# Performance work log

Measured on AMD Instinct MI355X. Metric: run time of the kernel, lower is better.

The kernel has to match this reference:

```python
import jax, jax.numpy as jnp
import numpy as np

N_NODES = 50000
N_EDGES = 600000
IN_F = 128
OUT_F = 128
SMALL = max(IN_F // 10, 1)  # floor(128/10) = 12
D_K = np.sqrt(SMALL).astype(np.float32)


def setup_inputs() -> dict:
    key = jax.random.key(0)
    ks = jax.random.split(key, 10)
    node_data = jax.random.normal(ks[0], (N_NODES, IN_F), dtype=jnp.float32)
    src = jax.random.randint(ks[1], (N_EDGES,), 0, N_NODES, dtype=jnp.int32)
    dst = jax.random.randint(ks[2], (N_EDGES,), 0, N_NODES, dtype=jnp.int32)
    s_q = 1.0 / np.sqrt(IN_F)
    Wq = jax.random.uniform(ks[3], (SMALL, IN_F), jnp.float32, -s_q, s_q)
    bq = jax.random.uniform(ks[4], (SMALL,), jnp.float32, -s_q, s_q)
    Wk = jax.random.uniform(ks[5], (SMALL, IN_F), jnp.float32, -s_q, s_q)
    bk = jax.random.uniform(ks[6], (SMALL,), jnp.float32, -s_q, s_q)
    W1 = jax.random.uniform(ks[7], (OUT_F, IN_F), jnp.float32, -s_q, s_q)
    W2 = jax.random.uniform(ks[8], (OUT_F, IN_F), jnp.float32, -s_q, s_q)
    b2 = jax.random.uniform(ks[9], (OUT_F,), jnp.float32, -s_q, s_q)
    return {"node_data": node_data, "src": src, "dst": dst,
            "Wq": Wq, "bq": bq, "Wk": Wk, "bk": bk,
            "W1": W1, "W2": W2, "b2": b2}


def reference(node_data, src, dst, Wq, bq, Wk, bk, W1, W2, b2):
    N = node_data.shape[0]
    # dgl.add_self_loop: append (i, i) for every node -> each dst has >= 1 edge
    loops = jnp.arange(N, dtype=src.dtype)
    s = jnp.concatenate([src, loops])
    d = jnp.concatenate([dst, loops])

    # query = Tanh(Linear), key = Linear  (shapes [N, SMALL])
    q = jnp.tanh(node_data @ Wq.T + bq)
    k = node_data @ Wk.T + bk

    # per-edge score: sum(query[src] * key[dst]) / sqrt(small)
    scores = jnp.sum(q[s] * k[d], axis=1) / D_K  # [E]

    # softmax over incoming edges of each dst node (segment softmax)
    seg_max = jax.ops.segment_max(scores, d, num_segments=N)
    w = jnp.exp(scores - seg_max[d])
    seg_sum = jax.ops.segment_sum(w, d, num_segments=N)
    w = w / seg_sum[d]  # [E]

    # weighted scatter-aggregate of src node inputs -> [N, IN_F]
    att = jax.ops.segment_sum(w[:, None] * node_data[s], d, num_segments=N)

    # DeepSetLayer: layer1(node_data) + layer2(node attention)
    x = node_data @ W1.T + (att @ W2.T + b2)
    # per-row L2 ('fro' over dim=1) normalization, then ReLU
    x = x / jnp.linalg.norm(x, axis=1, keepdims=True)
    return jax.nn.relu(x)
```

## Files before the change

### kernel.cpp

```cpp
#include <hip/hip_runtime.h>
#include <hip/hip_bf16.h>
#include <math.h>
#include <stdint.h>


#define IN_F 128
#define SMALL 12
#define QK_PAD 16
#define SCAN_ITEMS 8
#define SCAN_CHUNK 2048

typedef __attribute__((ext_vector_type(8))) _Float16 half8;
typedef __attribute__((ext_vector_type(4))) float f32x4;

__device__ __forceinline__ float dot12(const float* __restrict__ qrow,
                                       float4 c0, float4 c1, float4 c2) {
    float4 a = ((const float4*)qrow)[0];
    float4 b = ((const float4*)qrow)[1];
    float4 c = ((const float4*)qrow)[2];
    return a.x*c0.x + a.y*c0.y + a.z*c0.z + a.w*c0.w
         + b.x*c1.x + b.y*c1.y + b.z*c1.z + b.w*c1.w
         + c.x*c2.x + c.y*c2.y + c.z*c2.z + c.w*c2.w;
}

__device__ __forceinline__ half8 ld_h8(const float* p) {
    float4 x0 = *(const float4*)p;
    float4 x1 = *(const float4*)(p + 4);
    half8 a;
    a[0] = (_Float16)x0.x; a[1] = (_Float16)x0.y;
    a[2] = (_Float16)x0.z; a[3] = (_Float16)x0.w;
    a[4] = (_Float16)x1.x; a[5] = (_Float16)x1.y;
    a[6] = (_Float16)x1.z; a[7] = (_Float16)x1.w;
    return a;
}

__global__ __launch_bounds__(256) void prep_kernel(
    const float* __restrict__ nd,
    const float* __restrict__ Wq, const float* __restrict__ bq,
    const float* __restrict__ Wk, const float* __restrict__ bk,
    const int* __restrict__ dst,
    const float* __restrict__ W1, const float* __restrict__ W2,
    float* __restrict__ q, float* __restrict__ kf,
    unsigned short* __restrict__ ndb, int* __restrict__ cnt,
    unsigned short* __restrict__ rank, unsigned short* __restrict__ Wc,
    int N, int E, int NBQK, int NBCNT)
{
    int t = threadIdx.x;
    int b = blockIdx.x;

    if (b < NBQK) {
        int wv = t >> 6;
        int lane = t & 63;
        int col = lane & 15;
        int quad = lane >> 4;
        int tbase = b * 64 + wv * 16;

        int arow = tbase + col;
        int rowc = (arow < N) ? arow : (N - 1);
        const float* ap = nd + (size_t)rowc * IN_F + quad * 8;
        unsigned short* np = ndb + (size_t)arow * IN_F + quad * 8;

        const float* w0 = ((col < 12) ? (Wq + (size_t)col * IN_F)
                                      : (Wk + (size_t)(col - 12) * IN_F)) + quad * 8;
        const float* w1 = Wk + (size_t)((col < 8) ? (col + 4) : 4) * IN_F + quad * 8;
        bool hasw1 = (col < 8);

        half8 zero = {};
        f32x4 acc0 = (f32x4)0.f, acc1 = (f32x4)0.f;
#pragma unroll
        for (int ks = 0; ks < 4; ks++) {
            int k0 = ks * 32;
            half8 a = ld_h8(ap + k0);
            if (arow < N) *(half8*)(np + k0) = a;
            half8 bb0 = ld_h8(w0 + k0);
            half8 bb1 = hasw1 ? ld_h8(w1 + k0) : zero;
            acc0 = __builtin_amdgcn_mfma_f32_16x16x32_f16(a, bb0, acc0, 0, 0, 0);
            acc1 = __builtin_amdgcn_mfma_f32_16x16x32_f16(a, bb1, acc1, 0, 0, 0);
        }
        float bias0 = (col < 12) ? bq[col] : bk[col - 12];
        float bias1 = (col < 8) ? bk[col + 4] : 0.f;
#pragma unroll
        for (int r = 0; r < 4; r++) {
            int node = tbase + quad * 4 + r;
            if (node < N) {
                float v0 = acc0[r] + bias0;
                if (col < 12) q[(size_t)node * QK_PAD + col] = tanhf(v0);
                else          kf[(size_t)node * QK_PAD + (col - 12)] = v0;
                if (hasw1)    kf[(size_t)node * QK_PAD + col + 4] = acc1[r] + bias1;
            }
        }
    } else if (b < NBQK + NBCNT) {
        int ET = E + N;
        int stride = NBCNT * 256;
        for (int i = (b - NBQK) * 256 + t; i < ET; i += stride) {
            int d = (i < E) ? dst[i] : (i - E);
            rank[i] = (unsigned short)atomicAdd(&cnt[d], 1);
        }
    } else {
        int idx = (b - NBQK - NBCNT) * 256 + t;
        int f = idx >> 8, k = idx & 255;
        float v = (k < 128) ? W1[f * 128 + k] : W2[f * 128 + (k - 128)];
        ((_Float16*)Wc)[idx] = (_Float16)v;
    }
}

__global__ __launch_bounds__(256) void scan_local_kernel(
    int* __restrict__ off, int* __restrict__ bsum, int N)
{
    __shared__ int tsum[256];
    int t = threadIdx.x;
    int base = blockIdx.x * SCAN_CHUNK + t * SCAN_ITEMS;
    int v[SCAN_ITEMS];
    int s = 0;
#pragma unroll
    for (int i = 0; i < SCAN_ITEMS; i++) {
        int idx = base + i;
        v[i] = (idx < N) ? off[idx] : 0;
        s += v[i];
    }
    tsum[t] = s;
    __syncthreads();
    for (int d = 1; d < 256; d <<= 1) {
        int x = (t >= d) ? tsum[t - d] : 0;
        __syncthreads();
        tsum[t] += x;
        __syncthreads();
    }
    int excl = (t == 0) ? 0 : tsum[t - 1];
#pragma unroll
    for (int i = 0; i < SCAN_ITEMS; i++) {
        int idx = base + i;
        if (idx < N) off[idx] = excl;
        excl += v[i];
    }
    if (t == 255) bsum[blockIdx.x] = tsum[255];
}

__global__ __launch_bounds__(256) void scan_add_kernel(
    int* __restrict__ off, const int* __restrict__ bsum, int N, int NB)
{
    __shared__ int pre2[2];
    int t = threadIdx.x;
    if (t == 0) {
        int p = 0, tot = 0;
        for (int i = 0; i < NB; i++) {
            int v = bsum[i];
            if (i < (int)blockIdx.x) p += v;
            tot += v;
        }
        pre2[0] = p; pre2[1] = tot;
    }
    __syncthreads();
    int add = pre2[0];
    if (blockIdx.x == 0 && t == 0) off[N] = pre2[1];

    int base = blockIdx.x * SCAN_CHUNK + t * SCAN_ITEMS;
#pragma unroll
    for (int i = 0; i < SCAN_ITEMS; i++) {
        int j = base + i;
        if (j < N) off[j] += add;
    }
}

__global__ __launch_bounds__(256) void scatter_kernel(
    const int* __restrict__ src, const int* __restrict__ dst,
    const int* __restrict__ off, const unsigned short* __restrict__ rank,
    unsigned short* __restrict__ esrc, int E, int N)
{
    int i = blockIdx.x * 256 + threadIdx.x;
    if (i >= E + N) return;
    int d, s;
    if (i < E) { d = dst[i]; s = src[i]; }
    else       { d = i - E; s = d; }
    esrc[off[d] + (int)rank[i]] = (unsigned short)s;
}

__global__ __launch_bounds__(256) void attn_kernel(
    const unsigned short* __restrict__ ndb, const float* __restrict__ q,
    const float* __restrict__ kf, const int* __restrict__ off,
    const unsigned short* __restrict__ esrc, float* __restrict__ att, int N)
{
    const float INVDK = 0.28867513459481287f;
    int t = threadIdx.x;
    int lane = t & 63;
    int l16 = lane & 15;
    int gbase = lane & 48;
    int wid = blockIdx.x * 16 + (t >> 4);
    if (wid >= N) return;

    int start = off[wid];
    int deg = off[wid + 1] - start;

    const float4* kp = (const float4*)(kf + (size_t)wid * QK_PAD);
    float4 c0 = kp[0], c1 = kp[1], c2 = kp[2];

    float acc[8];
#pragma unroll
    for (int j = 0; j < 8; j++) acc[j] = 0.f;
    float inv;

    const unsigned short* nb = ndb + l16 * 8;

#define ACCUM(hv, ww) do {                                                    \
        acc[0] += (ww) * (float)(hv)[0]; acc[1] += (ww) * (float)(hv)[1];     \
        acc[2] += (ww) * (float)(hv)[2]; acc[3] += (ww) * (float)(hv)[3];     \
        acc[4] += (ww) * (float)(hv)[4]; acc[5] += (ww) * (float)(hv)[5];     \
        acc[6] += (ww) * (float)(hv)[6]; acc[7] += (ww) * (float)(hv)[7];     \
    } while (0)

    if (deg <= 16) {
        int si = 0;
        if (l16 < deg) si = (int)esrc[start + l16];

        int r0 = __shfl(si, gbase | 0);
        int r1 = __shfl(si, gbase | 1);
        int r2 = __shfl(si, gbase | 2);
        int r3 = __shfl(si, gbase | 3);
        half8 v0 = *(const half8*)(nb + (size_t)r0 * IN_F);
        half8 v1 = *(const half8*)(nb + (size_t)r1 * IN_F);
        half8 v2 = *(const half8*)(nb + (size_t)r2 * IN_F);
        half8 v3 = *(const half8*)(nb + (size_t)r3 * IN_F);

        float sc = -INFINITY;
        if (l16 < deg)
            sc = dot12(q + (size_t)si * QK_PAD, c0, c1, c2) * INVDK;
        float m = sc;
#pragma unroll
        for (int o = 8; o > 0; o >>= 1) m = fmaxf(m, __shfl_xor(m, o));
        float w = (l16 < deg) ? __expf(sc - m) : 0.f;
        float ls = w;
#pragma unroll
        for (int o = 8; o > 0; o >>= 1) ls += __shfl_xor(ls, o);
        inv = 1.f / ls;

        float w0 = __shfl(w, gbase | 0);
        float w1 = __shfl(w, gbase | 1);
        float w2 = __shfl(w, gbase | 2);
        float w3 = __shfl(w, gbase | 3);
        ACCUM(v0, w0); ACCUM(v1, w1); ACCUM(v2, w2); ACCUM(v3, w3);

        int i = 4;
        for (; i + 4 <= deg; i += 4) {
            float u0 = __shfl(w, gbase | i);       int s0 = __shfl(si, gbase | i);
            float u1 = __shfl(w, gbase | (i + 1)); int s1 = __shfl(si, gbase | (i + 1));
            float u2 = __shfl(w, gbase | (i + 2)); int s2 = __shfl(si, gbase | (i + 2));
            float u3 = __shfl(w, gbase | (i + 3)); int s3 = __shfl(si, gbase | (i + 3));
            half8 x0 = *(const half8*)(nb + (size_t)s0 * IN_F);
            half8 x1 = *(const half8*)(nb + (size_t)s1 * IN_F);
            half8 x2 = *(const half8*)(nb + (size_t)s2 * IN_F);
            half8 x3 = *(const half8*)(nb + (size_t)s3 * IN_F);
            ACCUM(x0, u0); ACCUM(x1, u1); ACCUM(x2, u2); ACCUM(x3, u3);
        }
        for (; i < deg; i++) {
            float wi = __shfl(w, gbase | i);
            int ri = __shfl(si, gbase | i);
            half8 x = *(const half8*)(nb + (size_t)ri * IN_F);
            ACCUM(x, wi);
        }
    } else {
        float m = -INFINITY;
        for (int i = l16; i < deg; i += 16) {
            int s2 = (int)esrc[start + i];
            m = fmaxf(m, dot12(q + (size_t)s2 * QK_PAD, c0, c1, c2) * INVDK);
        }
#pragma unroll
        for (int o = 8; o > 0; o >>= 1) m = fmaxf(m, __shfl_xor(m, o));
        float ls = 0.f;
        for (int i = l16; i < deg; i += 16) {
            int s2 = (int)esrc[start + i];
            ls += __expf(dot12(q + (size_t)s2 * QK_PAD, c0, c1, c2) * INVDK - m);
        }
#pragma unroll
        for (int o = 8; o > 0; o >>= 1) ls += __shfl_xor(ls, o);
        inv = 1.f / ls;

        for (int base2 = 0; base2 < deg; base2 += 16) {
            int cnt2 = deg - base2; if (cnt2 > 16) cnt2 = 16;
            float w = 0.f; int si = 0;
            if (l16 < cnt2) {
                si = (int)esrc[start + base2 + l16];
                w = __expf(dot12(q + (size_t)si * QK_PAD, c0, c1, c2) * INVDK - m);
            }
            int i = 0;
            for (; i + 4 <= cnt2; i += 4) {
                float u0 = __shfl(w, gbase | i);       int s0 = __shfl(si, gbase | i);
                float u1 = __shfl(w, gbase | (i + 1)); int s1 = __shfl(si, gbase | (i + 1));
                float u2 = __shfl(w, gbase | (i + 2)); int s2 = __shfl(si, gbase | (i + 2));
                float u3 = __shfl(w, gbase | (i + 3)); int s3 = __shfl(si, gbase | (i + 3));
                half8 x0 = *(const half8*)(nb + (size_t)s0 * IN_F);
                half8 x1 = *(const half8*)(nb + (size_t)s1 * IN_F);
                half8 x2 = *(const half8*)(nb + (size_t)s2 * IN_F);
                half8 x3 = *(const half8*)(nb + (size_t)s3 * IN_F);
                ACCUM(x0, u0); ACCUM(x1, u1); ACCUM(x2, u2); ACCUM(x3, u3);
            }
            for (; i < cnt2; i++) {
                float wi = __shfl(w, gbase | i);
                int ri = __shfl(si, gbase | i);
                half8 x = *(const half8*)(nb + (size_t)ri * IN_F);
                ACCUM(x, wi);
            }
        }
    }
#undef ACCUM

    float* op = att + (size_t)wid * IN_F + l16 * 8;
    float4 s0, s1;
    s0.x = acc[0] * inv; s0.y = acc[1] * inv; s0.z = acc[2] * inv; s0.w = acc[3] * inv;
    s1.x = acc[4] * inv; s1.y = acc[5] * inv; s1.z = acc[6] * inv; s1.w = acc[7] * inv;
    *(float4*)op = s0;
    *(float4*)(op + 4) = s1;
}

__global__ __launch_bounds__(256) void final_kernel(
    const unsigned short* __restrict__ ndb, const float* __restrict__ nd,
    const float* __restrict__ att,
    const unsigned short* __restrict__ Wc, const float* __restrict__ b2,
    float* __restrict__ out, int N)
{
    int wv = threadIdx.x >> 6;
    int lane = threadIdx.x & 63;
    int col = lane & 15;
    int quad = lane >> 4;

    int arow = blockIdx.x * 64 + wv * 16 + col;
    int rowc = (arow < N) ? arow : (N - 1);
    const unsigned short* a0p = ndb + (size_t)rowc * IN_F + quad * 8;
    const float* a1p = ((arow < N) ? att : nd) + (size_t)rowc * IN_F + quad * 8;

    f32x4 acc[8];
#pragma unroll
    for (int i = 0; i < 8; i++) acc[i] = (f32x4)0.f;

#pragma unroll
    for (int ks = 0; ks < 8; ks++) {
        int k0 = ks * 32;
        half8 a;
        if (ks < 4) a = *(const half8*)(a0p + k0);
        else        a = ld_h8(a1p + (k0 - 128));
#pragma unroll
        for (int ft = 0; ft < 8; ft++) {
            int n = ft * 16 + col;
            half8 bb = *(const half8*)(Wc + (size_t)n * 256 + k0 + quad * 8);
            acc[ft] = __builtin_amdgcn_mfma_f32_16x16x32_f16(a, bb, acc[ft], 0, 0, 0);
        }
    }

    float bias[8];
#pragma unroll
    for (int ft = 0; ft < 8; ft++) bias[ft] = b2[ft * 16 + col];

#pragma unroll
    for (int r = 0; r < 4; r++) {
        int node = blockIdx.x * 64 + wv * 16 + quad * 4 + r;
        float v[8];
        float ps = 0.f;
#pragma unroll
        for (int ft = 0; ft < 8; ft++) {
            v[ft] = acc[ft][r] + bias[ft];
            ps += v[ft] * v[ft];
        }
        ps += __shfl_xor(ps, 1);
        ps += __shfl_xor(ps, 2);
        ps += __shfl_xor(ps, 4);
        ps += __shfl_xor(ps, 8);
        float rn = rsqrtf(ps);
        if (node < N) {
            float* op = out + (size_t)node * 128 + col;
#pragma unroll
            for (int ft = 0; ft < 8; ft++)
                op[ft * 16] = fmaxf(v[ft] * rn, 0.f);
        }
    }
}

static inline char* align_up(char* p, size_t a) {
    return (char*)(((uintptr_t)p + (a - 1)) & ~(uintptr_t)(a - 1));
}

extern "C" void kernel_launch(void* const* d_in, const int* in_sizes, int n_in,
                              void* d_out, int out_size, void* d_ws, size_t ws_size,
                              hipStream_t stream) {
    const float* node_data = (const float*)d_in[0];
    const int*   src       = (const int*)d_in[1];
    const int*   dst       = (const int*)d_in[2];
    const float* Wq        = (const float*)d_in[3];
    const float* bq        = (const float*)d_in[4];
    const float* Wk        = (const float*)d_in[5];
    const float* bk        = (const float*)d_in[6];
    const float* W1        = (const float*)d_in[7];
    const float* W2        = (const float*)d_in[8];
    const float* b2        = (const float*)d_in[9];
    float* out = (float*)d_out;

    int N = in_sizes[0] / IN_F;
    int E = in_sizes[1];
    int ET = E + N;
    int NB = (N + SCAN_CHUNK - 1) / SCAN_CHUNK;
    int NBQK = (N + 63) / 64;
    int NBCNT = 512;
    int NBCVT = 128;

    char* w = (char*)d_ws;
    float* q  = (float*)w;  w += (size_t)N * QK_PAD * sizeof(float);
    float* kf = (float*)w;  w += (size_t)N * QK_PAD * sizeof(float);
    w = align_up(w, 256);
    unsigned short* ndb = (unsigned short*)w;  w += (size_t)N * IN_F * sizeof(unsigned short);
    w = align_up(w, 256);
    unsigned short* Wc = (unsigned short*)w;  w += 128 * 256 * sizeof(unsigned short);
    int* off  = (int*)w;  w += (size_t)(N + 1) * sizeof(int);
    int* bsum = (int*)w;  w += 256 * sizeof(int);
    unsigned short* rank = (unsigned short*)w;  w += (size_t)ET * sizeof(unsigned short);
    w = align_up(w, 256);
    unsigned short* esrc = (unsigned short*)w;  w += (size_t)ET * sizeof(unsigned short);
    float* att = out;

    hipMemsetAsync(off, 0, (size_t)(N + 1) * sizeof(int), stream);

    prep_kernel<<<NBQK + NBCNT + NBCVT, 256, 0, stream>>>(
        node_data, Wq, bq, Wk, bk, dst, W1, W2,
        q, kf, ndb, off, rank, Wc, N, E, NBQK, NBCNT);
    scan_local_kernel<<<NB, 256, 0, stream>>>(off, bsum, N);
    scan_add_kernel<<<NB, 256, 0, stream>>>(off, bsum, N, NB);
    scatter_kernel<<<(ET + 255) / 256, 256, 0, stream>>>(src, dst, off, rank, esrc, E, N);
    attn_kernel<<<(N + 15) / 16, 256, 0, stream>>>(ndb, q, kf, off, esrc, att, N);
    final_kernel<<<(N + 63) / 64, 256, 0, stream>>>(ndb, node_data, att, Wc, b2, out, N);
}
```

Measured before the change: 221.5 us.

## Pad CSR segments to 8, batch neighbor gathers, store attention in fp16

Keeps per-node counts in a separate array and pads each CSR segment to a multiple of 8. This allows source indices to be read as aligned 8-wide vectors and row gathers to be issued 8 or 16 at a time, for degree up to 32. It also writes the attention aggregate to an fp16 workspace buffer when the workspace is large enough, which halves that intermediate's traffic and removes the fp32-to-fp16 conversion in the final GEMM. The cost is a larger esrc buffer, extra register pressure from the wide batched loads, and some added precision loss in the attention aggregate.

```diff
diff --git a/kernel.cpp b/kernel.cpp
--- a/kernel.cpp
+++ b/kernel.cpp
@@ -11,6 +11,7 @@
 #define SCAN_CHUNK 2048
 
 typedef __attribute__((ext_vector_type(8))) _Float16 half8;
+typedef __attribute__((ext_vector_type(8))) unsigned short ushort8;
 typedef __attribute__((ext_vector_type(4))) float f32x4;
 
 __device__ __forceinline__ float dot12(const float* __restrict__ qrow,
@@ -105,7 +106,8 @@
 }
 
 __global__ __launch_bounds__(256) void scan_local_kernel(
-    int* __restrict__ off, int* __restrict__ bsum, int N)
+    const int* __restrict__ cnt, int* __restrict__ off,
+    int* __restrict__ bsum, int N)
 {
     __shared__ int tsum[256];
     int t = threadIdx.x;
@@ -115,7 +117,7 @@
 #pragma unroll
     for (int i = 0; i < SCAN_ITEMS; i++) {
         int idx = base + i;
-        v[i] = (idx < N) ? off[idx] : 0;
+        v[i] = (idx < N) ? ((cnt[idx] + 7) & ~7) : 0;
         s += v[i];
     }
     tsum[t] = s;
@@ -178,7 +180,8 @@
 __global__ __launch_bounds__(256) void attn_kernel(
     const unsigned short* __restrict__ ndb, const float* __restrict__ q,
     const float* __restrict__ kf, const int* __restrict__ off,
-    const unsigned short* __restrict__ esrc, float* __restrict__ att, int N)
+    const int* __restrict__ cnt, const unsigned short* __restrict__ esrc,
+    void* __restrict__ attv, int att16, int N)
 {
     const float INVDK = 0.28867513459481287f;
     int t = threadIdx.x;
@@ -189,7 +192,7 @@
     if (wid >= N) return;
 
     int start = off[wid];
-    int deg = off[wid + 1] - start;
+    int deg = cnt[wid];
 
     const float4* kp = (const float4*)(kf + (size_t)wid * QK_PAD);
     float4 c0 = kp[0], c1 = kp[1], c2 = kp[2];
@@ -208,54 +211,80 @@
         acc[6] += (ww) * (float)(hv)[6]; acc[7] += (ww) * (float)(hv)[7];     \
     } while (0)
 
-    if (deg <= 16) {
-        int si = 0;
-        if (l16 < deg) si = (int)esrc[start + l16];
-
-        int r0 = __shfl(si, gbase | 0);
-        int r1 = __shfl(si, gbase | 1);
-        int r2 = __shfl(si, gbase | 2);
-        int r3 = __shfl(si, gbase | 3);
-        half8 v0 = *(const half8*)(nb + (size_t)r0 * IN_F);
-        half8 v1 = *(const half8*)(nb + (size_t)r1 * IN_F);
-        half8 v2 = *(const half8*)(nb + (size_t)r2 * IN_F);
-        half8 v3 = *(const half8*)(nb + (size_t)r3 * IN_F);
-
+#define LOAD8(pfx, id)                                                        \
+    half8 pfx##0 = *(const half8*)(nb + (size_t)(id)[0] * IN_F);              \
+    half8 pfx##1 = *(const half8*)(nb + (size_t)(id)[1] * IN_F);              \
+    half8 pfx##2 = *(const half8*)(nb + (size_t)(id)[2] * IN_F);              \
+    half8 pfx##3 = *(const half8*)(nb + (size_t)(id)[3] * IN_F);              \
+    half8 pfx##4 = *(const half8*)(nb + (size_t)(id)[4] * IN_F);              \
+    half8 pfx##5 = *(const half8*)(nb + (size_t)(id)[5] * IN_F);              \
+    half8 pfx##6 = *(const half8*)(nb + (size_t)(id)[6] * IN_F);              \
+    half8 pfx##7 = *(const half8*)(nb + (size_t)(id)[7] * IN_F)
+
+#define SHFL8(wsrc, base)                                                     \
+    do { _Pragma("unroll")                                                    \
+         for (int _i = 0; _i < 8; _i++) wa[_i] = __shfl((wsrc), gbase | ((base) + _i)); } while (0)
+
+#define ACCUM8(pfx) do {                                                      \
+        ACCUM(pfx##0, wa[0]); ACCUM(pfx##1, wa[1]);                           \
+        ACCUM(pfx##2, wa[2]); ACCUM(pfx##3, wa[3]);                           \
+        ACCUM(pfx##4, wa[4]); ACCUM(pfx##5, wa[5]);                           \
+        ACCUM(pfx##6, wa[6]); ACCUM(pfx##7, wa[7]); } while (0)
+
+    if (deg <= 32) {
+        ushort8 pk0 = *(const ushort8*)(esrc + start);
+        ushort8 pk1 = *(const ushort8*)(esrc + start + 8);
+
+        int id0[8];
+#pragma unroll
+        for (int i = 0; i < 8; i++) id0[i] = (i < deg) ? (int)pk0[i] : 0;
+        LOAD8(v, id0);
+
+        int si = (int)esrc[start + l16];
         float sc = -INFINITY;
         if (l16 < deg)
             sc = dot12(q + (size_t)si * QK_PAD, c0, c1, c2) * INVDK;
-        float m = sc;
+        float sc1 = -INFINITY;
+        if (deg > 16) {
+            int si1 = (int)esrc[start + 16 + l16];
+            if (16 + l16 < deg)
+                sc1 = dot12(q + (size_t)si1 * QK_PAD, c0, c1, c2) * INVDK;
+        }
+        float m = fmaxf(sc, sc1);
 #pragma unroll
         for (int o = 8; o > 0; o >>= 1) m = fmaxf(m, __shfl_xor(m, o));
-        float w = (l16 < deg) ? __expf(sc - m) : 0.f;
-        float ls = w;
+        float w  = (l16 < deg)      ? __expf(sc - m)  : 0.f;
+        float w1 = (16 + l16 < deg) ? __expf(sc1 - m) : 0.f;
+        float ls = w + w1;
 #pragma unroll
         for (int o = 8; o > 0; o >>= 1) ls += __shfl_xor(ls, o);
         inv = 1.f / ls;
 
-        float w0 = __shfl(w, gbase | 0);
-        float w1 = __shfl(w, gbase | 1);
-        float w2 = __shfl(w, gbase | 2);
-        float w3 = __shfl(w, gbase | 3);
-        ACCUM(v0, w0); ACCUM(v1, w1); ACCUM(v2, w2); ACCUM(v3, w3);
-
-        int i = 4;
-        for (; i + 4 <= deg; i += 4) {
-            float u0 = __shfl(w, gbase | i);       int s0 = __shfl(si, gbase | i);
-            float u1 = __shfl(w, gbase | (i + 1)); int s1 = __shfl(si, gbase | (i + 1));
-            float u2 = __shfl(w, gbase | (i + 2)); int s2 = __shfl(si, gbase | (i + 2));
-            float u3 = __shfl(w, gbase | (i + 3)); int s3 = __shfl(si, gbase | (i + 3));
-            half8 x0 = *(const half8*)(nb + (size_t)s0 * IN_F);
-            half8 x1 = *(const half8*)(nb + (size_t)s1 * IN_F);
-            half8 x2 = *(const half8*)(nb + (size_t)s2 * IN_F);
-            half8 x3 = *(const half8*)(nb + (size_t)s3 * IN_F);
-            ACCUM(x0, u0); ACCUM(x1, u1); ACCUM(x2, u2); ACCUM(x3, u3);
-        }
-        for (; i < deg; i++) {
-            float wi = __shfl(w, gbase | i);
-            int ri = __shfl(si, gbase | i);
-            half8 x = *(const half8*)(nb + (size_t)ri * IN_F);
-            ACCUM(x, wi);
+        int id1[8];
+#pragma unroll
+        for (int i = 0; i < 8; i++) id1[i] = (8 + i < deg) ? (int)pk1[i] : 0;
+        LOAD8(u, id1);
+
+        float wa[8];
+        SHFL8(w, 0);
+        ACCUM8(v);
+        SHFL8(w, 8);
+        ACCUM8(u);
+
+        if (deg > 16) {
+            ushort8 pk2 = *(const ushort8*)(esrc + start + 16);
+            ushort8 pk3 = *(const ushort8*)(esrc + start + 24);
+            int id2[8], id3[8];
+#pragma unroll
+            for (int i = 0; i < 8; i++) id2[i] = (16 + i < deg) ? (int)pk2[i] : 0;
+#pragma unroll
+            for (int i = 0; i < 8; i++) id3[i] = (24 + i < deg) ? (int)pk3[i] : 0;
+            LOAD8(x, id2);
+            LOAD8(y, id3);
+            SHFL8(w1, 0);
+            ACCUM8(x);
+            SHFL8(w1, 8);
+            ACCUM8(y);
         }
     } else {
         float m = -INFINITY;
@@ -301,19 +330,30 @@
             }
         }
     }
+#undef ACCUM8
+#undef SHFL8
+#undef LOAD8
 #undef ACCUM
 
-    float* op = att + (size_t)wid * IN_F + l16 * 8;
-    float4 s0, s1;
-    s0.x = acc[0] * inv; s0.y = acc[1] * inv; s0.z = acc[2] * inv; s0.w = acc[3] * inv;
-    s1.x = acc[4] * inv; s1.y = acc[5] * inv; s1.z = acc[6] * inv; s1.w = acc[7] * inv;
-    *(float4*)op = s0;
-    *(float4*)(op + 4) = s1;
+    if (att16) {
+        unsigned short* op = (unsigned short*)attv + (size_t)wid * IN_F + l16 * 8;
+        half8 st;
+#pragma unroll
+        for (int j = 0; j < 8; j++) st[j] = (_Float16)(acc[j] * inv);
+        *(half8*)op = st;
+    } else {
+        float* op = (float*)attv + (size_t)wid * IN_F + l16 * 8;
+        float4 s0, s1;
+        s0.x = acc[0] * inv; s0.y = acc[1] * inv; s0.z = acc[2] * inv; s0.w = acc[3] * inv;
+        s1.x = acc[4] * inv; s1.y = acc[5] * inv; s1.z = acc[6] * inv; s1.w = acc[7] * inv;
+        *(float4*)op = s0;
+        *(float4*)(op + 4) = s1;
+    }
 }
 
 __global__ __launch_bounds__(256) void final_kernel(
     const unsigned short* __restrict__ ndb, const float* __restrict__ nd,
-    const float* __restrict__ att,
+    const void* __restrict__ attv, int att16,
     const unsigned short* __restrict__ Wc, const float* __restrict__ b2,
     float* __restrict__ out, int N)
 {
@@ -325,7 +365,8 @@
     int arow = blockIdx.x * 64 + wv * 16 + col;
     int rowc = (arow < N) ? arow : (N - 1);
     const unsigned short* a0p = ndb + (size_t)rowc * IN_F + quad * 8;
-    const float* a1p = ((arow < N) ? att : nd) + (size_t)rowc * IN_F + quad * 8;
+    const unsigned short* a1h = (const unsigned short*)attv + (size_t)rowc * IN_F + quad * 8;
+    const float* a1f = ((arow < N) ? (const float*)attv : nd) + (size_t)rowc * IN_F + quad * 8;
 
     f32x4 acc[8];
 #pragma unroll
@@ -335,8 +376,9 @@
     for (int ks = 0; ks < 8; ks++) {
         int k0 = ks * 32;
         half8 a;
-        if (ks < 4) a = *(const half8*)(a0p + k0);
-        else        a = ld_h8(a1p + (k0 - 128));
+        if (ks < 4)      a = *(const half8*)(a0p + k0);
+        else if (att16)  a = *(const half8*)(a1h + (k0 - 128));
+        else             a = ld_h8(a1f + (k0 - 128));
 #pragma unroll
         for (int ft = 0; ft < 8; ft++) {
             int n = ft * 16 + col;
@@ -395,6 +437,7 @@
     int N = in_sizes[0] / IN_F;
     int E = in_sizes[1];
     int ET = E + N;
+    int EPAD = E + 8 * N + 64;
     int NB = (N + SCAN_CHUNK - 1) / SCAN_CHUNK;
     int NBQK = (N + 63) / 64;
     int NBCNT = 512;
@@ -407,21 +450,29 @@
     unsigned short* ndb = (unsigned short*)w;  w += (size_t)N * IN_F * sizeof(unsigned short);
     w = align_up(w, 256);
     unsigned short* Wc = (unsigned short*)w;  w += 128 * 256 * sizeof(unsigned short);
+    int* cnt  = (int*)w;  w += (size_t)N * sizeof(int);
     int* off  = (int*)w;  w += (size_t)(N + 1) * sizeof(int);
     int* bsum = (int*)w;  w += 256 * sizeof(int);
     unsigned short* rank = (unsigned short*)w;  w += (size_t)ET * sizeof(unsigned short);
     w = align_up(w, 256);
-    unsigned short* esrc = (unsigned short*)w;  w += (size_t)ET * sizeof(unsigned short);
-    float* att = out;
-
-    hipMemsetAsync(off, 0, (size_t)(N + 1) * sizeof(int), stream);
+    unsigned short* esrc = (unsigned short*)w;  w += (size_t)EPAD * sizeof(unsigned short);
+
+    w = align_up(w, 256);
+    int att16 = 0;
+    void* attp = out;
+    if ((size_t)(w - (char*)d_ws) + (size_t)N * IN_F * sizeof(unsigned short) <= ws_size) {
+        att16 = 1;
+        attp = w;
+    }
+
+    hipMemsetAsync(cnt, 0, (size_t)N * sizeof(int), stream);
 
     prep_kernel<<<NBQK + NBCNT + NBCVT, 256, 0, stream>>>(
         node_data, Wq, bq, Wk, bk, dst, W1, W2,
-        q, kf, ndb, off, rank, Wc, N, E, NBQK, NBCNT);
-    scan_local_kernel<<<NB, 256, 0, stream>>>(off, bsum, N);
+        q, kf, ndb, cnt, rank, Wc, N, E, NBQK, NBCNT);
+    scan_local_kernel<<<NB, 256, 0, stream>>>(cnt, off, bsum, N);
     scan_add_kernel<<<NB, 256, 0, stream>>>(off, bsum, N, NB);
     scatter_kernel<<<(ET + 255) / 256, 256, 0, stream>>>(src, dst, off, rank, esrc, E, N);
-    attn_kernel<<<(N + 15) / 16, 256, 0, stream>>>(ndb, q, kf, off, esrc, att, N);
-    final_kernel<<<(N + 63) / 64, 256, 0, stream>>>(ndb, node_data, att, Wc, b2, out, N);
-}
+    attn_kernel<<<(N + 15) / 16, 256, 0, stream>>>(ndb, q, kf, off, cnt, esrc, attp, att16, N);
+    final_kernel<<<(N + 63) / 64, 256, 0, stream>>>(ndb, node_data, attp, att16, Wc, b2, out, N);
+}
```

Measured after the change: 207.5 us. 6.3% less time.
